# Optimization experiments

Measured on AMD Instinct MI355X. Metric: run time of the kernel, lower is better.

The kernel has to match this reference:

```python
import jax, jax.numpy as jnp
import numpy as np

B, S, E, H, T, VOCAB = 64, 512, 256, 512, 32, 32000

def setup_inputs():
    key = jax.random.key(0)
    ks = jax.random.split(key, 19)
    g = lambda i, shape: jax.random.normal(ks[i], shape, jnp.float32) * 0.05
    return {
        "sentence": jax.random.randint(ks[0], (S, B), 0, VOCAB),
        "emb_enc": g(1, (VOCAB, E)),
        "emb_dec": g(2, (VOCAB, E)),
        "W_ih": g(3, (4 * H, E)),
        "W_hh": g(4, (4 * H, H)),
        "b_ih": g(5, (4 * H,)),
        "b_hh": g(6, (4 * H,)),
        "dec_in0": g(7, (E,)),
        "Wx": g(8, (4 * H, E)),
        "bx": g(9, (4 * H,)),
        "Wh": g(10, (4 * H, H)),
        "bh": g(11, (4 * H,)),
        "W_out": g(12, (H, 2 * H)),
        "b_out": g(13, (H,)),
        "W_in": g(14, (H, H)),
        "b_in": g(15, (H,)),
        "W_ctx": g(16, (H, H)),
        "b_ctx": g(17, (H,)),
        "V": jax.random.uniform(ks[18], (H,), jnp.float32, -1.0, 1.0),
    }

def _lstm_cell(x, h, c, Wi, Whh, bi, bhh):
    # gate order i, f, g, o (matches torch LSTM and the decoder's chunk order)
    gates = x @ Wi.T + h @ Whh.T + bi + bhh
    i, f, g, o = jnp.split(gates, 4, axis=-1)
    c_t = jax.nn.sigmoid(f) * c + jax.nn.sigmoid(i) * jnp.tanh(g)
    h_t = jax.nn.sigmoid(o) * jnp.tanh(c_t)
    return h_t, c_t

def _pointer_net(sentence, emb_enc, emb_dec, W_ih, W_hh, b_ih, b_hh, dec_in0,
                 Wx, bx, Wh, bh, W_out, b_out, W_in, b_in, W_ctx, b_ctx, V):
    s_len, b = sentence.shape
    h_dim = W_hh.shape[1]
    embs = emb_enc[sentence]                          # [S, B, E]
    h0 = jnp.zeros((b, h_dim), embs.dtype)
    c0 = jnp.zeros((b, h_dim), embs.dtype)

    def enc_step(carry, x_t):
        h, c = _lstm_cell(x_t, carry[0], carry[1], W_ih, W_hh, b_ih, b_hh)
        return (h, c), h

    (h_n, c_n), enc_out = jax.lax.scan(enc_step, (h0, c0), embs)   # enc_out [S, B, H]
    context = enc_out.transpose(1, 0, 2)              # [B, S, H]
    # conv1d(kernel=1) projection of the context; constant across decode steps
    ctx = jnp.einsum('bsh,gh->bgs', context, W_ctx) + b_ctx[None, :, None]  # [B, H, S]

    dec_embs = emb_dec[sentence].transpose(1, 0, 2)   # [B, S, E]
    pos = jnp.arange(s_len)

    def dec_step(carry, _):
        dec_in, h, c, mask = carry
        h_t, c_t = _lstm_cell(dec_in, h, c, Wx, Wh, bx, bh)
        inp = h_t @ W_in.T + b_in                      # [B, H]
        att = jnp.einsum('h,bhs->bs', V, jnp.tanh(inp[:, :, None] + ctx))
        att = jnp.where(mask == 0, -jnp.inf, att)
        alpha = jax.nn.softmax(att, axis=1)            # [B, S]
        hidden_state = jnp.einsum('bhs,bs->bh', ctx, alpha)
        h_new = jnp.tanh(jnp.concatenate([hidden_state, h_t], axis=1) @ W_out.T + b_out)
        idx = jnp.argmax(alpha * mask, axis=1)         # greedy pointer, first max on ties
        one_hot = (pos[None, :] == idx[:, None]).astype(alpha.dtype)
        mask_new = mask * (1.0 - one_hot)
        next_in = jnp.take_along_axis(dec_embs, idx[:, None, None], axis=1)[:, 0, :]
        return (next_in, h_new, c_t, mask_new), (alpha, idx)

    mask0 = jnp.ones((b, s_len), embs.dtype)
    dec_in0_b = jnp.broadcast_to(dec_in0, (b, dec_in0.shape[0]))
    _, (alphas, ptrs) = jax.lax.scan(dec_step, (dec_in0_b, h_n, c_n, mask0), None, length=T)
    return alphas.transpose(1, 0, 2), ptrs.T          # [B, T, S], [B, T]

def reference(sentence, emb_enc, emb_dec, W_ih, W_hh, b_ih, b_hh, dec_in0,
              Wx, bx, Wh, bh, W_out, b_out, W_in, b_in, W_ctx, b_ctx, V):
    return _pointer_net(sentence, emb_enc, emb_dec, W_ih, W_hh, b_ih, b_hh, dec_in0,
                        Wx, bx, Wh, bh, W_out, b_out, W_in, b_in, W_ctx, b_ctx, V)
```

## Files before the change

### kernel.cpp

```cpp
#include <hip/hip_runtime.h>
#include <hip/hip_bf16.h>


typedef unsigned short u16;
typedef __bf16 bf16_t;
typedef bf16_t bf16x8 __attribute__((ext_vector_type(8)));
typedef float f32x4 __attribute__((ext_vector_type(4)));

#define MFMA16(a, b, c) __builtin_amdgcn_mfma_f32_16x16x32_bf16(a, b, c, 0, 0, 0)
#define AGENT __HIP_MEMORY_SCOPE_AGENT

#define FLG_OFF   64u
#define GENE_OFF  128u
#define LDE_OFF   192u
#define FLE_OFF   1216u
#define GEND_OFF  11456u
#define LDD_OFF   11520u
#define FLD_OFF   12544u
#define BAR_END   28928u
#define HE_OFF    32768u
#define CW_OFF    294912u
#define HD_OFF    425984u
#define AO_OFF    557056u
#define INP_OFF   819200u
#define ATT_OFF   950272u
#define MSK_OFF   1081344u
#define PAC_OFF   1212416u
#define PML_OFF   1736704u
#define DIN_OFF   1740800u
#define CTX_OFF   2097152u
#define CTXL_OFF  (CTX_OFF + 33554432u)
#define NEED_T0   (CTX_OFF + 67108864u)
#define NEED_T1   (CTX_OFF + 50331648u)
#define NEED_T2   (CTX_OFF + 33554432u)

__device__ __forceinline__ float bf2f(u16 b) {
  union { unsigned u; float f; } c; c.u = ((unsigned)b) << 16; return c.f;
}
__device__ __forceinline__ u16 f2bf(float x) {
  union { float f; unsigned u; } c; c.f = x;
  unsigned r = c.u + 0x7FFFu + ((c.u >> 16) & 1u);
  return (u16)(r >> 16);
}
__device__ __forceinline__ float sigf(float x) { return 1.0f / (1.0f + expf(-x)); }
__device__ __forceinline__ float sel4(float a0, float a1, float a2, float a3, int j) {
  float r = (j == 1) ? a1 : a0;
  r = (j == 2) ? a2 : r;
  r = (j == 3) ? a3 : r;
  return r;
}
__device__ __forceinline__ float wget(const void* p, long i, int f32m) {
  return f32m ? ((const float*)p)[i] : bf2f(((const u16*)p)[i]);
}
__device__ __forceinline__ void ld8(const void* p, long i, int f32m, float (&o)[8]) {
  if (f32m) {
    const float4* q = (const float4*)((const float*)p + i);
    float4 a = q[0], b = q[1];
    o[0] = a.x; o[1] = a.y; o[2] = a.z; o[3] = a.w;
    o[4] = b.x; o[5] = b.y; o[6] = b.z; o[7] = b.w;
  } else {
    uint4 u = *(const uint4*)((const u16*)p + i);
    unsigned ww[4] = {u.x, u.y, u.z, u.w};
#pragma unroll
    for (int k = 0; k < 4; ++k) {
      o[2 * k] = bf2f((u16)(ww[k] & 0xFFFFu));
      o[2 * k + 1] = bf2f((u16)(ww[k] >> 16));
    }
  }
}
__device__ __forceinline__ float ald(const float* p) {
  return __hip_atomic_load(p, __ATOMIC_RELAXED, AGENT);
}
__device__ __forceinline__ void ast(float* p, float v) {
  __hip_atomic_store(p, v, __ATOMIC_RELAXED, AGENT);
}
__device__ __forceinline__ void ld8T(const float* T, int kb, int bA, float (&o)[8]) {
  const float* p = T + kb * 64 + bA;
#pragma unroll
  for (int j = 0; j < 8; ++j) o[j] = ald(p + j * 64);
}

__device__ __forceinline__ void split3(float x, u16& h, u16& l, u16& l2) {
  union { float f; unsigned u; } c; c.f = x;
  h = (u16)(c.u >> 16);
  float r = x - bf2f(h);
  union { float f; unsigned u; } e; e.f = r;
  l = (u16)(e.u >> 16);
  float r2 = r - bf2f(l);
  union { float f; unsigned u; } g; g.f = r2;
  l2 = (u16)(g.u >> 16);
}
struct A3 { bf16x8 h, l, l2; };
__device__ __forceinline__ A3 split8(const float (&a)[8]) {
  A3 o;
#pragma unroll
  for (int j = 0; j < 8; ++j) {
    u16 h, l, l2;
    split3(a[j], h, l, l2);
    union { u16 u; bf16_t b; } ch, cl, c2;
    ch.u = h; cl.u = l; c2.u = l2;
    o.h[j] = ch.b; o.l[j] = cl.b; o.l2[j] = c2.b;
  }
  return o;
}
__device__ __forceinline__ f32x4 mfma6(const A3& a, const bf16x8& bh, const bf16x8& bl,
                                       const bf16x8& bl2, f32x4 acc) {
  acc = MFMA16(a.h, bh, acc);
  acc = MFMA16(a.l, bh, acc);
  acc = MFMA16(a.h, bl, acc);
  acc = MFMA16(a.l, bl, acc);
  acc = MFMA16(a.h, bl2, acc);
  acc = MFMA16(a.l2, bh, acc);
  return acc;
}
__device__ __forceinline__ f32x4 groupMM(const float (&a8)[8], const u16* B3c, int bo,
                                         f32x4 acc) {
  A3 a = split8(a8);
  return mfma6(a, *(const bf16x8*)(B3c + bo), *(const bf16x8*)(B3c + 4224 + bo),
               *(const bf16x8*)(B3c + 8448 + bo), acc);
}
__device__ __forceinline__ void stage16(u16* B3, const void* W, int f32m,
                                        long src, int n, int k16) {
  float t0[8], t1[8];
  ld8(W, src, f32m, t0);
  ld8(W, src + 8, f32m, t1);
#pragma unroll
  for (int j = 0; j < 8; ++j) {
    u16 h, l, l2; split3(t0[j], h, l, l2);
    int o = n * 264 + k16 + j;
    B3[o] = h; B3[4224 + o] = l; B3[8448 + o] = l2;
  }
#pragma unroll
  for (int j = 0; j < 8; ++j) {
    u16 h, l, l2; split3(t1[j], h, l, l2);
    int o = n * 264 + k16 + 8 + j;
    B3[o] = h; B3[4224 + o] = l; B3[8448 + o] = l2;
  }
}

__device__ __forceinline__ void ctx_store(char* ws, int tier, int oi, float x) {
  if (tier == 0) { ((float*)(ws + CTX_OFF))[oi] = x; return; }
  if (tier >= 3) return;
  u16 hi = f2bf(x);
  ((u16*)(ws + CTX_OFF))[oi] = hi;
  if (tier == 1) {
    unsigned e = hi & 0x7F80u; if (e == 0) e = 0x0080u;
    float us = bf2f((u16)e) * 0.00390625f;
    float r = (x - bf2f(hi)) / us;
    int q = (int)__float2int_rn(r * 254.0f);
    q = max(-127, min(127, q));
    ((signed char*)(ws + CTXL_OFF))[oi] = (signed char)q;
  }
}
__device__ __forceinline__ void ctx_load8(const char* ws, int tier, int oi, float (&cx)[8]) {
  if (tier == 0) {
    const float4* p = (const float4*)((const float*)(ws + CTX_OFF) + oi);
    float4 a = p[0], b = p[1];
    cx[0] = a.x; cx[1] = a.y; cx[2] = a.z; cx[3] = a.w;
    cx[4] = b.x; cx[5] = b.y; cx[6] = b.z; cx[7] = b.w;
    return;
  }
  if (tier >= 3) {
#pragma unroll
    for (int j = 0; j < 8; ++j) cx[j] = 0.0f;
    return;
  }
  uint4 hu = *(const uint4*)((const u16*)(ws + CTX_OFF) + oi);
  unsigned hw[4] = {hu.x, hu.y, hu.z, hu.w};
  u16 h[8];
#pragma unroll
  for (int k = 0; k < 4; ++k) { h[2*k] = (u16)(hw[k] & 0xFFFFu); h[2*k+1] = (u16)(hw[k] >> 16); }
#pragma unroll
  for (int j = 0; j < 8; ++j) cx[j] = bf2f(h[j]);
  if (tier == 1) {
    const signed char* lp = (const signed char*)(ws + CTXL_OFF) + oi;
#pragma unroll
    for (int j = 0; j < 8; ++j) {
      unsigned e = h[j] & 0x7F80u; if (e == 0) e = 0x0080u;
      float us = bf2f((u16)e) * 0.00390625f;
      cx[j] += (float)lp[j] * us * (1.0f / 254.0f);
    }
  }
}

__device__ __forceinline__ void sbar(char* ws, unsigned flOff, unsigned ldOff,
                                     unsigned genOff, int wg, int nwg, int gen) {
  __builtin_amdgcn_s_waitcnt(0);
  __syncthreads();
  const int tid = threadIdx.x;
  if (tid < 64) {
    int* fl = (int*)(ws + flOff);
    int* ldv = (int*)(ws + ldOff);
    int* gp = (int*)(ws + genOff);
    if (tid == 0) __hip_atomic_store(&fl[wg * 16], gen, __ATOMIC_RELAXED, AGENT);
    const int mem = nwg >> 4;
    if (wg < 16) {
      if (tid < mem) {
        const int* f = &fl[(wg + (tid << 4)) * 16];
        while (__hip_atomic_load(f, __ATOMIC_RELAXED, AGENT) < gen)
          __builtin_amdgcn_s_sleep(2);
      }
      if (tid == 0) __hip_atomic_store(&ldv[wg * 16], gen, __ATOMIC_RELAXED, AGENT);
    }
    if (wg == 0) {
      if (tid < 16) {
        const int* f = &ldv[tid * 16];
        while (__hip_atomic_load(f, __ATOMIC_RELAXED, AGENT) < gen)
          __builtin_amdgcn_s_sleep(2);
      }
      if (tid == 0) __hip_atomic_store(gp, gen, __ATOMIC_RELAXED, AGENT);
    }
    if (tid == 0)
      while (__hip_atomic_load((const int*)gp, __ATOMIC_RELAXED, AGENT) < gen)
        __builtin_amdgcn_s_sleep(2);
  }
  __syncthreads();
}

__global__ void prep_detect(const void* embE, char* ws) {
  __shared__ int cnt;
  if (threadIdx.x == 0) cnt = 0;
  __syncthreads();
  const u16* p = (const u16*)embE;
  int c = 0;
  for (int i = threadIdx.x; i < 4096; i += 256) {
    float v = bf2f(p[i]);
    if (!(fabsf(v) < 4.0f)) c++;
  }
  atomicAdd(&cnt, c);
  __syncthreads();
  if (threadIdx.x == 0) *(int*)(ws + FLG_OFF) = (cnt > 200) ? 1 : 0;
}

__global__ void prep_init(const void* din0, char* ws) {
  const int f32m = *(const int*)(ws + FLG_OFF);
  int i0 = blockIdx.x * 256 + threadIdx.x;
  int stride = gridDim.x * 256;
  int* bars = (int*)ws;
  for (int i = i0; i < (int)((BAR_END - GENE_OFF) / 4); i += stride)
    bars[(GENE_OFF / 4) + i] = 0;
  float* h0 = (float*)(ws + HE_OFF);
  float* mask = (float*)(ws + MSK_OFF);
  float* dinT = (float*)(ws + DIN_OFF);
  for (int i = i0; i < 32768; i += stride) { h0[i] = 0.0f; mask[i] = 1.0f; }
  for (int i = i0; i < 16384; i += stride) dinT[i] = wget(din0, i >> 6, f32m);
}

__global__ __launch_bounds__(256, 1) void enc_pers(
    const int* __restrict__ sent, const void* __restrict__ embE,
    const void* __restrict__ Wih, const void* __restrict__ Whh,
    const void* __restrict__ bih, const void* __restrict__ bhh,
    const void* __restrict__ Wctx, const void* __restrict__ bctx,
    char* __restrict__ ws, int tier) {
  __shared__ __align__(16) u16 B3[38016];
  const int tid = threadIdx.x, w = blockIdx.x;
  const int f32m = *(const int*)(ws + FLG_OFF);
  const int lane = tid & 63, v = tid >> 6, ln15 = lane & 15, q = lane >> 4;
  const int bA = v * 16 + ln15;
  const int sn = tid >> 4, sk = (tid & 15) * 16;
  float* heT = (float*)(ws + HE_OFF);
  float* cwp = (float*)(ws + CW_OFF);

  const int g = ln15 & 3;
  const int unit = w * 4 + (ln15 >> 2);
  float creg[4];
#pragma unroll
  for (int r = 0; r < 4; ++r) creg[r] = 0.0f;
  float bias = 0.0f;

  if (w < 128) {
    long grC = (long)(g * 512 + unit);
    bias = wget(bih, grC, f32m) + wget(bhh, grC, f32m);
    const long grS = (long)((sn & 3) * 512 + w * 4 + (sn >> 2));
    stage16(B3, Wih, f32m, grS * 256 + sk, sn, sk);
    stage16(B3 + 12672, Whh, f32m, grS * 512 + sk, sn, sk);
    stage16(B3 + 25344, Whh, f32m, grS * 512 + 256 + sk, sn, sk);
  } else {
    const long grS = (long)((w - 128) * 16 + sn);
    stage16(B3, Wctx, f32m, grS * 512 + sk, sn, sk);
    stage16(B3 + 12672, Wctx, f32m, grS * 512 + 256 + sk, sn, sk);
  }
  __syncthreads();

#pragma unroll 1
  for (int t = 0; t <= 512; ++t) {
    const int slot = t & 1;
    const float* hsT = heT + slot * 32768;
    if (w < 128) {
      if (t < 512) {
        const int tok = sent[t * 64 + bA];
        float aH[16][8];
#pragma unroll
        for (int kk = 0; kk < 16; ++kk) ld8T(hsT, kk * 32 + q * 8, bA, aH[kk]);
        float aE[8][8];
#pragma unroll
        for (int ks = 0; ks < 8; ++ks)
          ld8(embE, (long)tok * 256 + ks * 32 + q * 8, f32m, aE[ks]);
        f32x4 acc = {0.f, 0.f, 0.f, 0.f};
#pragma unroll
        for (int ks = 0; ks < 8; ++ks)
          acc = groupMM(aE[ks], B3, ln15 * 264 + ks * 32 + q * 8, acc);
#pragma unroll
        for (int kk = 0; kk < 16; ++kk)
          acc = groupMM(aH[kk], B3 + (1 + (kk >> 3)) * 12672,
                        ln15 * 264 + (kk & 7) * 32 + q * 8, acc);
        float* hdT = heT + (slot ^ 1) * 32768;
#pragma unroll
        for (int r = 0; r < 4; ++r) {
          int br = v * 16 + q * 4 + r;
          float val = acc[r] + bias;
          float x1 = __shfl_xor(val, 1);
          float x2 = __shfl_xor(val, 2);
          float x3 = __shfl_xor(val, 3);
          float gi = sel4(val, x1, x2, x3, g);
          float gf = sel4(val, x1, x2, x3, g ^ 1);
          float gg = sel4(val, x1, x2, x3, g ^ 2);
          float go = sel4(val, x1, x2, x3, g ^ 3);
          float cn = sigf(gf) * creg[r] + sigf(gi) * tanhf(gg);
          float hv = sigf(go) * tanhf(cn);
          creg[r] = cn;
          if (g == 0) ast(hdT + unit * 64 + br, hv);
        }
      }
    } else {
      if (t >= 1) {
        const int w2 = w - 128;
        float aH[16][8];
#pragma unroll
        for (int kk = 0; kk < 16; ++kk) ld8T(hsT, kk * 32 + q * 8, bA, aH[kk]);
        f32x4 acc = {0.f, 0.f, 0.f, 0.f};
#pragma unroll
        for (int kk = 0; kk < 16; ++kk)
          acc = groupMM(aH[kk], B3 + (kk >> 3) * 12672,
                        ln15 * 264 + (kk & 7) * 32 + q * 8, acc);
        const int d = w2 * 16 + ln15;
        float bb = wget(bctx, d, f32m);
#pragma unroll
        for (int r = 0; r < 4; ++r) {
          int br = v * 16 + q * 4 + r;
          ctx_store(ws, tier, (br * 512 + (t - 1)) * 512 + d, acc[r] + bb);
        }
      }
    }
    if (t < 512) sbar(ws, FLE_OFF, LDE_OFF, GENE_OFF, w, 160, t + 1);
  }
  if (w < 128 && g == 0) {
#pragma unroll
    for (int r = 0; r < 4; ++r) cwp[(v * 16 + q * 4 + r) * 512 + unit] = creg[r];
  }
}

__global__ __launch_bounds__(256, 1) void dec_pers(
    const int* __restrict__ sent, const void* __restrict__ embD,
    const void* __restrict__ Wx, const void* __restrict__ bx,
    const void* __restrict__ Wh, const void* __restrict__ bh,
    const void* __restrict__ Wout, const void* __restrict__ bout,
    const void* __restrict__ Win, const void* __restrict__ bin,
    const void* __restrict__ V, char* __restrict__ ws,
    float* __restrict__ out, int tier) {
  __shared__ __align__(16) u16 B3[50688];
  __shared__ float accL[512];
  __shared__ float mlL[8];
  __shared__ float redA[256];
  __shared__ int redI[256];

  const int tid = threadIdx.x, wg = blockIdx.x;
  const int f32m = *(const int*)(ws + FLG_OFF);
  const int lane = tid & 63, v = tid >> 6, ln15 = lane & 15, q = lane >> 4;
  const int bA = v * 16 + ln15;
  const int sn = tid >> 4, sk = (tid & 15) * 16;
  float* hdT = (float*)(ws + HD_OFF);
  float* aoT = (float*)(ws + AO_OFF);
  float* inp = (float*)(ws + INP_OFF);
  float* att = (float*)(ws + ATT_OFF);
  float* mask = (float*)(ws + MSK_OFF);
  float* pac = (float*)(ws + PAC_OFF);
  float* pml = (float*)(ws + PML_OFF);
  float* dinT = (float*)(ws + DIN_OFF);
  const float* hnT = (const float*)(ws + HE_OFF);
  int bgen = 0;

  const int g = ln15 & 3;
  const int unit = (wg < 128) ? (wg * 4 + (ln15 >> 2)) : 0;
  float creg[4];
  float bias = 0.0f;
  if (wg < 128) {
    const float* cwp = (const float*)(ws + CW_OFF);
#pragma unroll
    for (int r = 0; r < 4; ++r) creg[r] = cwp[(v * 16 + q * 4 + r) * 512 + unit];
    bias = wget(bx, (long)(g * 512 + unit), f32m) + wget(bh, (long)(g * 512 + unit), f32m);
  }
  float vj[8];
#pragma unroll
  for (int j = 0; j < 8; ++j) vj[j] = wget(V, lane * 8 + j, f32m);

  if (wg < 128) {
    const long grS = (long)((sn & 3) * 512 + wg * 4 + (sn >> 2));
    stage16(B3, Wx, f32m, grS * 256 + sk, sn, sk);
    stage16(B3 + 12672, Wh, f32m, grS * 512 + sk, sn, sk);
    stage16(B3 + 25344, Wh, f32m, grS * 512 + 256 + sk, sn, sk);
  } else if (wg < 160) {
    const long grS = (long)((wg - 128) * 16 + sn);
    stage16(B3, Win, f32m, grS * 512 + sk, sn, sk);
    stage16(B3 + 12672, Win, f32m, grS * 512 + 256 + sk, sn, sk);
  } else if (wg < 192) {
    const long grS = (long)((wg - 160) * 16 + sn);
#pragma unroll
    for (int cc = 0; cc < 4; ++cc)
      stage16(B3 + cc * 12672, Wout, f32m, grS * 1024 + cc * 256 + sk, sn, sk);
  }
  __syncthreads();

#pragma unroll 1
  for (int t = 0; t < 32; ++t) {
    if (wg < 128) {
      const float* hsT = (t == 0) ? hnT : hdT;
      float aH[16][8];
#pragma unroll
      for (int kk = 0; kk < 16; ++kk) ld8T(hsT, kk * 32 + q * 8, bA, aH[kk]);
      float aD[8][8];
#pragma unroll
      for (int ks = 0; ks < 8; ++ks) ld8T(dinT, ks * 32 + q * 8, bA, aD[ks]);
      f32x4 acc = {0.f, 0.f, 0.f, 0.f};
#pragma unroll
      for (int ks = 0; ks < 8; ++ks)
        acc = groupMM(aD[ks], B3, ln15 * 264 + ks * 32 + q * 8, acc);
#pragma unroll
      for (int kk = 0; kk < 16; ++kk)
        acc = groupMM(aH[kk], B3 + (1 + (kk >> 3)) * 12672,
                      ln15 * 264 + (kk & 7) * 32 + q * 8, acc);
#pragma unroll
      for (int r = 0; r < 4; ++r) {
        int br = v * 16 + q * 4 + r;
        float val = acc[r] + bias;
        float x1 = __shfl_xor(val, 1);
        float x2 = __shfl_xor(val, 2);
        float x3 = __shfl_xor(val, 3);
        float gi = sel4(val, x1, x2, x3, g);
        float gf = sel4(val, x1, x2, x3, g ^ 1);
        float gg = sel4(val, x1, x2, x3, g ^ 2);
        float go = sel4(val, x1, x2, x3, g ^ 3);
        float cn = sigf(gf) * creg[r] + sigf(gi) * tanhf(gg);
        float hv = sigf(go) * tanhf(cn);
        creg[r] = cn;
        if (g == 0) ast(aoT + (512 + unit) * 64 + br, hv);
      }
    }
    sbar(ws, FLD_OFF, LDD_OFF, GEND_OFF, wg, 256, ++bgen);
    if (wg >= 128 && wg < 160) {
      const int w = wg - 128;
      float aH[16][8];
#pragma unroll
      for (int kk = 0; kk < 16; ++kk) ld8T(aoT, 512 + kk * 32 + q * 8, bA, aH[kk]);
      f32x4 acc = {0.f, 0.f, 0.f, 0.f};
#pragma unroll
      for (int kk = 0; kk < 16; ++kk)
        acc = groupMM(aH[kk], B3 + (kk >> 3) * 12672,
                      ln15 * 264 + (kk & 7) * 32 + q * 8, acc);
      const int d = w * 16 + ln15;
      float bb = wget(bin, d, f32m);
#pragma unroll
      for (int r = 0; r < 4; ++r)
        ast(inp + (v * 16 + q * 4 + r) * 512 + d, acc[r] + bb);
    }
    sbar(ws, FLD_OFF, LDD_OFF, GEND_OFF, wg, 256, ++bgen);
    {
      const int b = wg & 63, qq = wg >> 6;
      float ij[8];
#pragma unroll
      for (int j = 0; j < 8; ++j) ij[j] = ald(inp + b * 512 + lane * 8 + j);
      for (int i = tid; i < 512; i += 256) accL[i] = 0.0f;
      __syncthreads();
      float m = -1e30f, l = 0.0f;
      float oacc[8];
#pragma unroll
      for (int j = 0; j < 8; ++j) oacc[j] = 0.0f;
      const int s0 = qq * 128 + v * 32;
      float mkC = ald(mask + b * 512 + s0);
      float cxC[8], cxN[8];
      ctx_load8(ws, tier, (b * 512 + s0) * 512 + lane * 8, cxC);
#pragma unroll 1
      for (int i0 = 0; i0 < 32; ++i0) {
        const int s = s0 + i0;
        float mkN = 0.0f;
        if (i0 < 31) {
          mkN = ald(mask + b * 512 + s + 1);
          ctx_load8(ws, tier, (b * 512 + s + 1) * 512 + lane * 8, cxN);
        }
        if (mkC == 0.0f) {
          if (lane == 0) ast(att + b * 512 + s, -1e30f);
        } else {
          float p = 0.0f;
#pragma unroll
          for (int j = 0; j < 8; ++j) p += vj[j] * tanhf(ij[j] + cxC[j]);
#pragma unroll
          for (int off = 1; off < 64; off <<= 1) p += __shfl_xor(p, off);
          if (lane == 0) ast(att + b * 512 + s, p);
          if (p <= m) {
            float e = expf(p - m);
            l += e;
#pragma unroll
            for (int j = 0; j < 8; ++j) oacc[j] += e * cxC[j];
          } else {
            float sc = expf(m - p);
            l = l * sc + 1.0f;
#pragma unroll
            for (int j = 0; j < 8; ++j) oacc[j] = oacc[j] * sc + cxC[j];
            m = p;
          }
        }
        mkC = mkN;
#pragma unroll
        for (int j = 0; j < 8; ++j) cxC[j] = cxN[j];
      }
      if (lane == 0) { mlL[v * 2] = m; mlL[v * 2 + 1] = l; }
      __syncthreads();
      float M = fmaxf(fmaxf(mlL[0], mlL[2]), fmaxf(mlL[4], mlL[6]));
      float Lq = 0.0f;
#pragma unroll
      for (int vv = 0; vv < 4; ++vv) Lq += mlL[vv * 2 + 1] * expf(mlL[vv * 2] - M);
      float scv = expf(m - M);
      for (int vv = 0; vv < 4; ++vv) {
        if (v == vv) {
#pragma unroll
          for (int j = 0; j < 8; ++j) accL[lane * 8 + j] += oacc[j] * scv;
        }
        __syncthreads();
      }
      for (int i = tid; i < 512; i += 256) ast(pac + (b * 4 + qq) * 512 + i, accL[i]);
      if (tid == 0) {
        ast(pml + (b * 4 + qq) * 2, M);
        ast(pml + (b * 4 + qq) * 2 + 1, Lq);
      }
    }
    sbar(ws, FLD_OFF, LDD_OFF, GEND_OFF, wg, 256, ++bgen);
    if (wg < 64) {
      const int bb = wg;
      float m0 = ald(pml + (bb * 4 + 0) * 2), m1 = ald(pml + (bb * 4 + 1) * 2);
      float m2 = ald(pml + (bb * 4 + 2) * 2), m3 = ald(pml + (bb * 4 + 3) * 2);
      float l0 = ald(pml + (bb * 4 + 0) * 2 + 1), l1 = ald(pml + (bb * 4 + 1) * 2 + 1);
      float l2 = ald(pml + (bb * 4 + 2) * 2 + 1), l3 = ald(pml + (bb * 4 + 3) * 2 + 1);
      float M = fmaxf(fmaxf(m0, m1), fmaxf(m2, m3));
      float e0 = expf(m0 - M), e1 = expf(m1 - M), e2 = expf(m2 - M), e3 = expf(m3 - M);
      float L = l0 * e0 + l1 * e1 + l2 * e2 + l3 * e3;
      L = fmaxf(L, 1e-30f);
      for (int h = tid; h < 512; h += 256) {
        float hv = (ald(pac + (bb * 4 + 0) * 512 + h) * e0 +
                    ald(pac + (bb * 4 + 1) * 512 + h) * e1 +
                    ald(pac + (bb * 4 + 2) * 512 + h) * e2 +
                    ald(pac + (bb * 4 + 3) * 512 + h) * e3) / L;
        ast(aoT + h * 64 + bb, hv);
      }
      float bestA = -1.0f;
      int bestS = 0;
#pragma unroll
      for (int k = 0; k < 2; ++k) {
        int s = tid * 2 + k;
        float a = expf(ald(att + bb * 512 + s) - M) / L;
        out[(bb * 32 + t) * 512 + s] = a;
        if (a > bestA) { bestA = a; bestS = s; }
      }
      redA[tid] = bestA;
      redI[tid] = bestS;
      __syncthreads();
      for (int st = 128; st > 0; st >>= 1) {
        if (tid < st) {
          if (redA[tid + st] > redA[tid]) { redA[tid] = redA[tid + st]; redI[tid] = redI[tid + st]; }
        }
        __syncthreads();
      }
      int idx = redI[0];
      if (tid == 0) {
        ast(mask + bb * 512 + idx, 0.0f);
        out[1048576 + bb * 32 + t] = (float)idx;
      }
      int token = sent[idx * 64 + bb];
      ast(dinT + tid * 64 + bb, wget(embD, (long)token * 256 + tid, f32m));
    }
    sbar(ws, FLD_OFF, LDD_OFF, GEND_OFF, wg, 256, ++bgen);
    if (wg >= 160 && wg < 192) {
      const int w = wg - 160;
      f32x4 acc = {0.f, 0.f, 0.f, 0.f};
      float aH[16][8];
#pragma unroll
      for (int kk = 0; kk < 16; ++kk) ld8T(aoT, kk * 32 + q * 8, bA, aH[kk]);
#pragma unroll
      for (int kk = 0; kk < 16; ++kk)
        acc = groupMM(aH[kk], B3 + (kk >> 3) * 12672,
                      ln15 * 264 + (kk & 7) * 32 + q * 8, acc);
#pragma unroll
      for (int kk = 0; kk < 16; ++kk) ld8T(aoT, 512 + kk * 32 + q * 8, bA, aH[kk]);
#pragma unroll
      for (int kk = 0; kk < 16; ++kk)
        acc = groupMM(aH[kk], B3 + (2 + (kk >> 3)) * 12672,
                      ln15 * 264 + (kk & 7) * 32 + q * 8, acc);
      const int d = w * 16 + ln15;
      float bb = wget(bout, d, f32m);
#pragma unroll
      for (int r = 0; r < 4; ++r)
        ast(hdT + d * 64 + (v * 16 + q * 4 + r), tanhf(acc[r] + bb));
    }
    sbar(ws, FLD_OFF, LDD_OFF, GEND_OFF, wg, 256, ++bgen);
  }
}

__global__ void diag_kernel(char* ws, float* out, int wsMiB) {
  if (threadIdx.x == 0 && blockIdx.x == 0) {
    int f = *(int*)(ws + FLG_OFF);
    out[0] = (float)(wsMiB + 2000 * f);
  }
}

extern "C" void kernel_launch(void* const* d_in, const int* in_sizes, int n_in,
                              void* d_out, int out_size, void* d_ws, size_t ws_size,
                              hipStream_t stream) {
  (void)in_sizes; (void)n_in; (void)out_size;
  const int* sent = (const int*)d_in[0];
  const void* embE = d_in[1];
  const void* embD = d_in[2];
  const void* Wih = d_in[3];
  const void* Whh = d_in[4];
  const void* bih = d_in[5];
  const void* bhh = d_in[6];
  const void* din0 = d_in[7];
  const void* Wx = d_in[8];
  const void* bx = d_in[9];
  const void* Wh = d_in[10];
  const void* bh = d_in[11];
  const void* Wout = d_in[12];
  const void* bout = d_in[13];
  const void* Win = d_in[14];
  const void* bin = d_in[15];
  const void* Wctx = d_in[16];
  const void* bctx = d_in[17];
  const void* V = d_in[18];
  char* ws = (char*)d_ws;
  float* out = (float*)d_out;

  int tier;
  if (ws_size >= (size_t)NEED_T0) tier = 0;
  else if (ws_size >= (size_t)NEED_T1) tier = 1;
  else if (ws_size >= (size_t)NEED_T2) tier = 2;
  else tier = 3;

  prep_detect<<<dim3(1), dim3(256), 0, stream>>>(embE, ws);
  prep_init<<<dim3(64), dim3(256), 0, stream>>>(din0, ws);
  enc_pers<<<dim3(160), dim3(256), 0, stream>>>(sent, embE, Wih, Whh, bih, bhh,
                                                Wctx, bctx, ws, tier);
  dec_pers<<<dim3(256), dim3(256), 0, stream>>>(sent, embD, Wx, bx, Wh, bh, Wout, bout,
                                                Win, bin, V, ws, out, tier);
  if (tier >= 2)
    diag_kernel<<<dim3(1), dim3(64), 0, stream>>>(ws, out, (int)(ws_size >> 20));
}
```

Measured before the change: 7.979 ms.

## Split grid barriers into arrive/wait and overlap input work with barrier latency

```diff
diff --git a/kernel.cpp b/kernel.cpp
--- a/kernel.cpp
+++ b/kernel.cpp
@@ -3,6 +3,7 @@
 
 
 typedef unsigned short u16;
+typedef unsigned long long u64;
 typedef __bf16 bf16_t;
 typedef bf16_t bf16x8 __attribute__((ext_vector_type(8)));
 typedef float f32x4 __attribute__((ext_vector_type(4)));
@@ -74,10 +75,17 @@
 __device__ __forceinline__ void ast(float* p, float v) {
   __hip_atomic_store(p, v, __ATOMIC_RELAXED, AGENT);
 }
-__device__ __forceinline__ void ld8T(const float* T, int kb, int bA, float (&o)[8]) {
-  const float* p = T + kb * 64 + bA;
-#pragma unroll
-  for (int j = 0; j < 8; ++j) o[j] = ald(p + j * 64);
+__device__ __forceinline__ int aldi(const int* p) {
+  return __hip_atomic_load(p, __ATOMIC_RELAXED, AGENT);
+}
+__device__ __forceinline__ void ld8c(const float* row, int off, float (&o)[8]) {
+  const u64* p = (const u64*)(row + off);
+#pragma unroll
+  for (int j = 0; j < 4; ++j) {
+    union { u64 u; float f[2]; } c;
+    c.u = __hip_atomic_load(p + j, __ATOMIC_RELAXED, AGENT);
+    o[2 * j] = c.f[0]; o[2 * j + 1] = c.f[1];
+  }
 }
 
 __device__ __forceinline__ void split3(float x, u16& h, u16& l, u16& l2) {
@@ -90,33 +98,43 @@
   union { float f; unsigned u; } g; g.f = r2;
   l2 = (u16)(g.u >> 16);
 }
-struct A3 { bf16x8 h, l, l2; };
-__device__ __forceinline__ A3 split8(const float (&a)[8]) {
-  A3 o;
-#pragma unroll
-  for (int j = 0; j < 8; ++j) {
-    u16 h, l, l2;
-    split3(a[j], h, l, l2);
-    union { u16 u; bf16_t b; } ch, cl, c2;
-    ch.u = h; cl.u = l; c2.u = l2;
-    o.h[j] = ch.b; o.l[j] = cl.b; o.l2[j] = c2.b;
-  }
-  return o;
-}
-__device__ __forceinline__ f32x4 mfma6(const A3& a, const bf16x8& bh, const bf16x8& bl,
-                                       const bf16x8& bl2, f32x4 acc) {
-  acc = MFMA16(a.h, bh, acc);
-  acc = MFMA16(a.l, bh, acc);
-  acc = MFMA16(a.h, bl, acc);
-  acc = MFMA16(a.l, bl, acc);
-  acc = MFMA16(a.h, bl2, acc);
-  acc = MFMA16(a.l2, bh, acc);
+__device__ __forceinline__ void split8v(const float (&a)[8], bf16x8& H, bf16x8& L,
+                                        bf16x8& L2) {
+  union { unsigned u[4]; bf16x8 v; } hh, ll, mm;
+#pragma unroll
+  for (int k = 0; k < 4; ++k) {
+    union { float f; unsigned u; } x0, x1;
+    x0.f = a[2 * k]; x1.f = a[2 * k + 1];
+    unsigned t0 = x0.u & 0xFFFF0000u, t1 = x1.u & 0xFFFF0000u;
+    union { unsigned u; float f; } b0, b1; b0.u = t0; b1.u = t1;
+    float r0 = x0.f - b0.f, r1 = x1.f - b1.f;
+    union { float f; unsigned u; } e0, e1; e0.f = r0; e1.f = r1;
+    unsigned s0 = e0.u & 0xFFFF0000u, s1 = e1.u & 0xFFFF0000u;
+    union { unsigned u; float f; } c0, c1; c0.u = s0; c1.u = s1;
+    float q0 = r0 - c0.f, q1 = r1 - c1.f;
+    union { float f; unsigned u; } g0, g1; g0.f = q0; g1.f = q1;
+    hh.u[k] = t1 | (x0.u >> 16);
+    ll.u[k] = s1 | (e0.u >> 16);
+    mm.u[k] = (g1.u & 0xFFFF0000u) | (g0.u >> 16);
+  }
+  H = hh.v; L = ll.v; L2 = mm.v;
+}
+__device__ __forceinline__ f32x4 mfma6(const bf16x8& ah, const bf16x8& al,
+                                       const bf16x8& al2, const bf16x8& bh,
+                                       const bf16x8& bl, const bf16x8& bl2, f32x4 acc) {
+  acc = MFMA16(ah, bh, acc);
+  acc = MFMA16(al, bh, acc);
+  acc = MFMA16(ah, bl, acc);
+  acc = MFMA16(al, bl, acc);
+  acc = MFMA16(ah, bl2, acc);
+  acc = MFMA16(al2, bh, acc);
   return acc;
 }
-__device__ __forceinline__ f32x4 groupMM(const float (&a8)[8], const u16* B3c, int bo,
-                                         f32x4 acc) {
-  A3 a = split8(a8);
-  return mfma6(a, *(const bf16x8*)(B3c + bo), *(const bf16x8*)(B3c + 4224 + bo),
+__device__ __forceinline__ f32x4 groupMMv(const float (&a8)[8], const u16* B3c, int bo,
+                                          f32x4 acc) {
+  bf16x8 H, L, L2;
+  split8v(a8, H, L, L2);
+  return mfma6(H, L, L2, *(const bf16x8*)(B3c + bo), *(const bf16x8*)(B3c + 4224 + bo),
                *(const bf16x8*)(B3c + 8448 + bo), acc);
 }
 __device__ __forceinline__ void stage16(u16* B3, const void* W, int f32m,
@@ -183,36 +201,36 @@
   }
 }
 
-__device__ __forceinline__ void sbar(char* ws, unsigned flOff, unsigned ldOff,
-                                     unsigned genOff, int wg, int nwg, int gen) {
+__device__ __forceinline__ void sbar_arrive(char* ws, unsigned flOff, int wg, int gen) {
   __builtin_amdgcn_s_waitcnt(0);
   __syncthreads();
+  if (threadIdx.x == 0)
+    __hip_atomic_store((int*)(ws + flOff) + wg * 16, gen, __ATOMIC_RELAXED, AGENT);
+}
+__device__ __forceinline__ void sbar_wait(char* ws, unsigned flOff, unsigned ldOff,
+                                          unsigned genOff, int wg, int nwg, int gen) {
   const int tid = threadIdx.x;
   if (tid < 64) {
     int* fl = (int*)(ws + flOff);
     int* ldv = (int*)(ws + ldOff);
     int* gp = (int*)(ws + genOff);
-    if (tid == 0) __hip_atomic_store(&fl[wg * 16], gen, __ATOMIC_RELAXED, AGENT);
     const int mem = nwg >> 4;
     if (wg < 16) {
       if (tid < mem) {
         const int* f = &fl[(wg + (tid << 4)) * 16];
-        while (__hip_atomic_load(f, __ATOMIC_RELAXED, AGENT) < gen)
-          __builtin_amdgcn_s_sleep(2);
+        while (aldi(f) < gen) __builtin_amdgcn_s_sleep(2);
       }
       if (tid == 0) __hip_atomic_store(&ldv[wg * 16], gen, __ATOMIC_RELAXED, AGENT);
     }
     if (wg == 0) {
       if (tid < 16) {
         const int* f = &ldv[tid * 16];
-        while (__hip_atomic_load(f, __ATOMIC_RELAXED, AGENT) < gen)
-          __builtin_amdgcn_s_sleep(2);
+        while (aldi(f) < gen) __builtin_amdgcn_s_sleep(2);
       }
       if (tid == 0) __hip_atomic_store(gp, gen, __ATOMIC_RELAXED, AGENT);
     }
     if (tid == 0)
-      while (__hip_atomic_load((const int*)gp, __ATOMIC_RELAXED, AGENT) < gen)
-        __builtin_amdgcn_s_sleep(2);
+      while (aldi((const int*)gp) < gen) __builtin_amdgcn_s_sleep(2);
   }
   __syncthreads();
 }
@@ -243,7 +261,7 @@
   float* mask = (float*)(ws + MSK_OFF);
   float* dinT = (float*)(ws + DIN_OFF);
   for (int i = i0; i < 32768; i += stride) { h0[i] = 0.0f; mask[i] = 1.0f; }
-  for (int i = i0; i < 16384; i += stride) dinT[i] = wget(din0, i >> 6, f32m);
+  for (int i = i0; i < 16384; i += stride) dinT[i] = wget(din0, i & 255, f32m);
 }
 
 __global__ __launch_bounds__(256, 1) void enc_pers(
@@ -283,57 +301,68 @@
   __syncthreads();
 
 #pragma unroll 1
-  for (int t = 0; t <= 512; ++t) {
+  for (int t = 0; t < 512; ++t) {
     const int slot = t & 1;
-    const float* hsT = heT + slot * 32768;
     if (w < 128) {
-      if (t < 512) {
-        const int tok = sent[t * 64 + bA];
-        float aH[16][8];
-#pragma unroll
-        for (int kk = 0; kk < 16; ++kk) ld8T(hsT, kk * 32 + q * 8, bA, aH[kk]);
-        float aE[8][8];
-#pragma unroll
-        for (int ks = 0; ks < 8; ++ks)
-          ld8(embE, (long)tok * 256 + ks * 32 + q * 8, f32m, aE[ks]);
+      const int tok = sent[t * 64 + bA];
+      f32x4 acc = {0.f, 0.f, 0.f, 0.f};
+      {
+        float aE[4][8];
+#pragma unroll
+        for (int pf = 0; pf < 3; ++pf)
+          ld8(embE, (long)tok * 256 + pf * 32 + q * 8, f32m, aE[pf]);
+#pragma unroll
+        for (int ks = 0; ks < 8; ++ks) {
+          if (ks + 3 < 8) ld8(embE, (long)tok * 256 + (ks + 3) * 32 + q * 8, f32m,
+                              aE[(ks + 3) & 3]);
+          acc = groupMMv(aE[ks & 3], B3, ln15 * 264 + ks * 32 + q * 8, acc);
+        }
+      }
+      if (t) sbar_wait(ws, FLE_OFF, LDE_OFF, GENE_OFF, w, 160, t);
+      {
+        const float* hrow = heT + slot * 32768 + bA * 512;
+        float aH[4][8];
+#pragma unroll
+        for (int pf = 0; pf < 3; ++pf) ld8c(hrow, pf * 32 + q * 8, aH[pf]);
+#pragma unroll
+        for (int kk = 0; kk < 16; ++kk) {
+          if (kk + 3 < 16) ld8c(hrow, (kk + 3) * 32 + q * 8, aH[(kk + 3) & 3]);
+          acc = groupMMv(aH[kk & 3], B3 + (1 + (kk >> 3)) * 12672,
+                         ln15 * 264 + (kk & 7) * 32 + q * 8, acc);
+        }
+      }
+      float* hdTs = heT + (slot ^ 1) * 32768;
+#pragma unroll
+      for (int r = 0; r < 4; ++r) {
+        int br = v * 16 + q * 4 + r;
+        float val = acc[r] + bias;
+        float x1 = __shfl_xor(val, 1);
+        float x2 = __shfl_xor(val, 2);
+        float x3 = __shfl_xor(val, 3);
+        float gi = sel4(val, x1, x2, x3, g);
+        float gf = sel4(val, x1, x2, x3, g ^ 1);
+        float gg = sel4(val, x1, x2, x3, g ^ 2);
+        float go = sel4(val, x1, x2, x3, g ^ 3);
+        float cn = sigf(gf) * creg[r] + sigf(gi) * tanhf(gg);
+        float hv = sigf(go) * tanhf(cn);
+        creg[r] = cn;
+        if (g == 0) ast(hdTs + br * 512 + unit, hv);
+      }
+    } else {
+      if (t) {
+        sbar_wait(ws, FLE_OFF, LDE_OFF, GENE_OFF, w, 160, t);
+        const float* hrow = heT + slot * 32768 + bA * 512;
+        float aH[4][8];
+#pragma unroll
+        for (int pf = 0; pf < 3; ++pf) ld8c(hrow, pf * 32 + q * 8, aH[pf]);
         f32x4 acc = {0.f, 0.f, 0.f, 0.f};
 #pragma unroll
-        for (int ks = 0; ks < 8; ++ks)
-          acc = groupMM(aE[ks], B3, ln15 * 264 + ks * 32 + q * 8, acc);
-#pragma unroll
-        for (int kk = 0; kk < 16; ++kk)
-          acc = groupMM(aH[kk], B3 + (1 + (kk >> 3)) * 12672,
-                        ln15 * 264 + (kk & 7) * 32 + q * 8, acc);
-        float* hdT = heT + (slot ^ 1) * 32768;
-#pragma unroll
-        for (int r = 0; r < 4; ++r) {
-          int br = v * 16 + q * 4 + r;
-          float val = acc[r] + bias;
-          float x1 = __shfl_xor(val, 1);
-          float x2 = __shfl_xor(val, 2);
-          float x3 = __shfl_xor(val, 3);
-          float gi = sel4(val, x1, x2, x3, g);
-          float gf = sel4(val, x1, x2, x3, g ^ 1);
-          float gg = sel4(val, x1, x2, x3, g ^ 2);
-          float go = sel4(val, x1, x2, x3, g ^ 3);
-          float cn = sigf(gf) * creg[r] + sigf(gi) * tanhf(gg);
-          float hv = sigf(go) * tanhf(cn);
-          creg[r] = cn;
-          if (g == 0) ast(hdT + unit * 64 + br, hv);
+        for (int kk = 0; kk < 16; ++kk) {
+          if (kk + 3 < 16) ld8c(hrow, (kk + 3) * 32 + q * 8, aH[(kk + 3) & 3]);
+          acc = groupMMv(aH[kk & 3], B3 + (kk >> 3) * 12672,
+                         ln15 * 264 + (kk & 7) * 32 + q * 8, acc);
         }
-      }
-    } else {
-      if (t >= 1) {
-        const int w2 = w - 128;
-        float aH[16][8];
-#pragma unroll
-        for (int kk = 0; kk < 16; ++kk) ld8T(hsT, kk * 32 + q * 8, bA, aH[kk]);
-        f32x4 acc = {0.f, 0.f, 0.f, 0.f};
-#pragma unroll
-        for (int kk = 0; kk < 16; ++kk)
-          acc = groupMM(aH[kk], B3 + (kk >> 3) * 12672,
-                        ln15 * 264 + (kk & 7) * 32 + q * 8, acc);
-        const int d = w2 * 16 + ln15;
+        const int d = (w - 128) * 16 + ln15;
         float bb = wget(bctx, d, f32m);
 #pragma unroll
         for (int r = 0; r < 4; ++r) {
@@ -342,9 +371,29 @@
         }
       }
     }
-    if (t < 512) sbar(ws, FLE_OFF, LDE_OFF, GENE_OFF, w, 160, t + 1);
-  }
-  if (w < 128 && g == 0) {
+    sbar_arrive(ws, FLE_OFF, w, t + 1);
+  }
+  sbar_wait(ws, FLE_OFF, LDE_OFF, GENE_OFF, w, 160, 512);
+  if (w >= 128) {
+    const float* hrow = heT + bA * 512;
+    float aH[4][8];
+#pragma unroll
+    for (int pf = 0; pf < 3; ++pf) ld8c(hrow, pf * 32 + q * 8, aH[pf]);
+    f32x4 acc = {0.f, 0.f, 0.f, 0.f};
+#pragma unroll
+    for (int kk = 0; kk < 16; ++kk) {
+      if (kk + 3 < 16) ld8c(hrow, (kk + 3) * 32 + q * 8, aH[(kk + 3) & 3]);
+      acc = groupMMv(aH[kk & 3], B3 + (kk >> 3) * 12672,
+                     ln15 * 264 + (kk & 7) * 32 + q * 8, acc);
+    }
+    const int d = (w - 128) * 16 + ln15;
+    float bb = wget(bctx, d, f32m);
+#pragma unroll
+    for (int r = 0; r < 4; ++r) {
+      int br = v * 16 + q * 4 + r;
+      ctx_store(ws, tier, (br * 512 + 511) * 512 + d, acc[r] + bb);
+    }
+  } else if (g == 0) {
 #pragma unroll
     for (int r = 0; r < 4; ++r) cwp[(v * 16 + q * 4 + r) * 512 + unit] = creg[r];
   }
@@ -411,28 +460,36 @@
   }
   __syncthreads();
 
+  f32x4 acc1 = {0.f, 0.f, 0.f, 0.f};
+  if (wg < 128) {
+    const float* drow = dinT + bA * 256;
+    float aD[4][8];
+#pragma unroll
+    for (int pf = 0; pf < 3; ++pf) ld8c(drow, pf * 32 + q * 8, aD[pf]);
+#pragma unroll
+    for (int ks = 0; ks < 8; ++ks) {
+      if (ks + 3 < 8) ld8c(drow, (ks + 3) * 32 + q * 8, aD[(ks + 3) & 3]);
+      acc1 = groupMMv(aD[ks & 3], B3, ln15 * 264 + ks * 32 + q * 8, acc1);
+    }
+  }
+
 #pragma unroll 1
   for (int t = 0; t < 32; ++t) {
     if (wg < 128) {
-      const float* hsT = (t == 0) ? hnT : hdT;
-      float aH[16][8];
-#pragma unroll
-      for (int kk = 0; kk < 16; ++kk) ld8T(hsT, kk * 32 + q * 8, bA, aH[kk]);
-      float aD[8][8];
-#pragma unroll
-      for (int ks = 0; ks < 8; ++ks) ld8T(dinT, ks * 32 + q * 8, bA, aD[ks]);
-      f32x4 acc = {0.f, 0.f, 0.f, 0.f};
-#pragma unroll
-      for (int ks = 0; ks < 8; ++ks)
-        acc = groupMM(aD[ks], B3, ln15 * 264 + ks * 32 + q * 8, acc);
-#pragma unroll
-      for (int kk = 0; kk < 16; ++kk)
-        acc = groupMM(aH[kk], B3 + (1 + (kk >> 3)) * 12672,
-                      ln15 * 264 + (kk & 7) * 32 + q * 8, acc);
+      const float* hrow = ((t == 0) ? hnT : (const float*)hdT) + bA * 512;
+      float aH[4][8];
+#pragma unroll
+      for (int pf = 0; pf < 3; ++pf) ld8c(hrow, pf * 32 + q * 8, aH[pf]);
+#pragma unroll
+      for (int kk = 0; kk < 16; ++kk) {
+        if (kk + 3 < 16) ld8c(hrow, (kk + 3) * 32 + q * 8, aH[(kk + 3) & 3]);
+        acc1 = groupMMv(aH[kk & 3], B3 + (1 + (kk >> 3)) * 12672,
+                        ln15 * 264 + (kk & 7) * 32 + q * 8, acc1);
+      }
 #pragma unroll
       for (int r = 0; r < 4; ++r) {
         int br = v * 16 + q * 4 + r;
-        float val = acc[r] + bias;
+        float val = acc1[r] + bias;
         float x1 = __shfl_xor(val, 1);
         float x2 = __shfl_xor(val, 2);
         float x3 = __shfl_xor(val, 3);
@@ -443,50 +500,60 @@
         float cn = sigf(gf) * creg[r] + sigf(gi) * tanhf(gg);
         float hv = sigf(go) * tanhf(cn);
         creg[r] = cn;
-        if (g == 0) ast(aoT + (512 + unit) * 64 + br, hv);
-      }
-    }
-    sbar(ws, FLD_OFF, LDD_OFF, GEND_OFF, wg, 256, ++bgen);
+        if (g == 0) ast(aoT + br * 1024 + 512 + unit, hv);
+      }
+    }
+    ++bgen;
+    sbar_arrive(ws, FLD_OFF, wg, bgen);
+    sbar_wait(ws, FLD_OFF, LDD_OFF, GEND_OFF, wg, 256, bgen);
     if (wg >= 128 && wg < 160) {
-      const int w = wg - 128;
-      float aH[16][8];
-#pragma unroll
-      for (int kk = 0; kk < 16; ++kk) ld8T(aoT, 512 + kk * 32 + q * 8, bA, aH[kk]);
+      const float* arow = aoT + bA * 1024;
+      float aH[4][8];
+#pragma unroll
+      for (int pf = 0; pf < 3; ++pf) ld8c(arow, 512 + pf * 32 + q * 8, aH[pf]);
       f32x4 acc = {0.f, 0.f, 0.f, 0.f};
 #pragma unroll
-      for (int kk = 0; kk < 16; ++kk)
-        acc = groupMM(aH[kk], B3 + (kk >> 3) * 12672,
-                      ln15 * 264 + (kk & 7) * 32 + q * 8, acc);
-      const int d = w * 16 + ln15;
+      for (int kk = 0; kk < 16; ++kk) {
+        if (kk + 3 < 16) ld8c(arow, 512 + (kk + 3) * 32 + q * 8, aH[(kk + 3) & 3]);
+        acc = groupMMv(aH[kk & 3], B3 + (kk >> 3) * 12672,
+                       ln15 * 264 + (kk & 7) * 32 + q * 8, acc);
+      }
+      const int d = (wg - 128) * 16 + ln15;
       float bb = wget(bin, d, f32m);
 #pragma unroll
       for (int r = 0; r < 4; ++r)
         ast(inp + (v * 16 + q * 4 + r) * 512 + d, acc[r] + bb);
     }
-    sbar(ws, FLD_OFF, LDD_OFF, GEND_OFF, wg, 256, ++bgen);
+    ++bgen;
+    sbar_arrive(ws, FLD_OFF, wg, bgen);
+    const int b = wg & 63, qq = wg >> 6;
+    const int s0 = qq * 128 + v * 32;
+    float mkB[4];
+    float cxB[4][8];
+#pragma unroll
+    for (int pf = 0; pf < 3; ++pf) {
+      mkB[pf] = ald(mask + b * 512 + s0 + pf);
+      ctx_load8(ws, tier, (b * 512 + s0 + pf) * 512 + lane * 8, cxB[pf]);
+    }
+    sbar_wait(ws, FLD_OFF, LDD_OFF, GEND_OFF, wg, 256, bgen);
     {
-      const int b = wg & 63, qq = wg >> 6;
       float ij[8];
-#pragma unroll
-      for (int j = 0; j < 8; ++j) ij[j] = ald(inp + b * 512 + lane * 8 + j);
+      ld8c(inp + b * 512, lane * 8, ij);
       for (int i = tid; i < 512; i += 256) accL[i] = 0.0f;
       __syncthreads();
       float m = -1e30f, l = 0.0f;
       float oacc[8];
 #pragma unroll
       for (int j = 0; j < 8; ++j) oacc[j] = 0.0f;
-      const int s0 = qq * 128 + v * 32;
-      float mkC = ald(mask + b * 512 + s0);
-      float cxC[8], cxN[8];
-      ctx_load8(ws, tier, (b * 512 + s0) * 512 + lane * 8, cxC);
 #pragma unroll 1
       for (int i0 = 0; i0 < 32; ++i0) {
         const int s = s0 + i0;
-        float mkN = 0.0f;
-        if (i0 < 31) {
-          mkN = ald(mask + b * 512 + s + 1);
-          ctx_load8(ws, tier, (b * 512 + s + 1) * 512 + lane * 8, cxN);
+        if (i0 + 3 < 32) {
+          mkB[(i0 + 3) & 3] = ald(mask + b * 512 + s + 3);
+          ctx_load8(ws, tier, (b * 512 + s + 3) * 512 + lane * 8, cxB[(i0 + 3) & 3]);
         }
+        float mkC = mkB[i0 & 3];
+        const float (&cxC)[8] = cxB[i0 & 3];
         if (mkC == 0.0f) {
           if (lane == 0) ast(att + b * 512 + s, -1e30f);
         } else {
@@ -509,9 +576,6 @@
             m = p;
           }
         }
-        mkC = mkN;
-#pragma unroll
-        for (int j = 0; j < 8; ++j) cxC[j] = cxN[j];
       }
       if (lane == 0) { mlL[v * 2] = m; mlL[v * 2 + 1] = l; }
       __syncthreads();
@@ -533,7 +597,9 @@
         ast(pml + (b * 4 + qq) * 2 + 1, Lq);
       }
     }
-    sbar(ws, FLD_OFF, LDD_OFF, GEND_OFF, wg, 256, ++bgen);
+    ++bgen;
+    sbar_arrive(ws, FLD_OFF, wg, bgen);
+    sbar_wait(ws, FLD_OFF, LDD_OFF, GEND_OFF, wg, 256, bgen);
     if (wg < 64) {
       const int bb = wg;
       float m0 = ald(pml + (bb * 4 + 0) * 2), m1 = ald(pml + (bb * 4 + 1) * 2);
@@ -549,7 +615,7 @@
                     ald(pac + (bb * 4 + 1) * 512 + h) * e1 +
                     ald(pac + (bb * 4 + 2) * 512 + h) * e2 +
                     ald(pac + (bb * 4 + 3) * 512 + h) * e3) / L;
-        ast(aoT + h * 64 + bb, hv);
+        ast(aoT + bb * 1024 + h, hv);
       }
       float bestA = -1.0f;
       int bestS = 0;
@@ -575,32 +641,45 @@
         out[1048576 + bb * 32 + t] = (float)idx;
       }
       int token = sent[idx * 64 + bb];
-      ast(dinT + tid * 64 + bb, wget(embD, (long)token * 256 + tid, f32m));
-    }
-    sbar(ws, FLD_OFF, LDD_OFF, GEND_OFF, wg, 256, ++bgen);
+      ast(dinT + bb * 256 + tid, wget(embD, (long)token * 256 + tid, f32m));
+    }
+    ++bgen;
+    sbar_arrive(ws, FLD_OFF, wg, bgen);
+    sbar_wait(ws, FLD_OFF, LDD_OFF, GEND_OFF, wg, 256, bgen);
     if (wg >= 160 && wg < 192) {
-      const int w = wg - 160;
+      const float* arow = aoT + bA * 1024;
+      float aH[4][8];
+#pragma unroll
+      for (int pf = 0; pf < 3; ++pf) ld8c(arow, pf * 32 + q * 8, aH[pf]);
       f32x4 acc = {0.f, 0.f, 0.f, 0.f};
-      float aH[16][8];
-#pragma unroll
-      for (int kk = 0; kk < 16; ++kk) ld8T(aoT, kk * 32 + q * 8, bA, aH[kk]);
-#pragma unroll
-      for (int kk = 0; kk < 16; ++kk)
-        acc = groupMM(aH[kk], B3 + (kk >> 3) * 12672,
-                      ln15 * 264 + (kk & 7) * 32 + q * 8, acc);
-#pragma unroll
-      for (int kk = 0; kk < 16; ++kk) ld8T(aoT, 512 + kk * 32 + q * 8, bA, aH[kk]);
-#pragma unroll
-      for (int kk = 0; kk < 16; ++kk)
-        acc = groupMM(aH[kk], B3 + (2 + (kk >> 3)) * 12672,
-                      ln15 * 264 + (kk & 7) * 32 + q * 8, acc);
-      const int d = w * 16 + ln15;
+#pragma unroll
+      for (int kk = 0; kk < 32; ++kk) {
+        if (kk + 3 < 32) ld8c(arow, (kk + 3) * 32 + q * 8, aH[(kk + 3) & 3]);
+        acc = groupMMv(aH[kk & 3], B3 + (kk >> 3) * 12672,
+                       ln15 * 264 + (kk & 7) * 32 + q * 8, acc);
+      }
+      const int d = (wg - 160) * 16 + ln15;
       float bb = wget(bout, d, f32m);
 #pragma unroll
       for (int r = 0; r < 4; ++r)
-        ast(hdT + d * 64 + (v * 16 + q * 4 + r), tanhf(acc[r] + bb));
-    }
-    sbar(ws, FLD_OFF, LDD_OFF, GEND_OFF, wg, 256, ++bgen);
+        ast(hdT + (v * 16 + q * 4 + r) * 512 + d, tanhf(acc[r] + bb));
+    }
+    ++bgen;
+    sbar_arrive(ws, FLD_OFF, wg, bgen);
+    if (wg < 128 && t < 31) {
+      const float* drow = dinT + bA * 256;
+      float aD[4][8];
+#pragma unroll
+      for (int pf = 0; pf < 3; ++pf) ld8c(drow, pf * 32 + q * 8, aD[pf]);
+      f32x4 accn = {0.f, 0.f, 0.f, 0.f};
+#pragma unroll
+      for (int ks = 0; ks < 8; ++ks) {
+        if (ks + 3 < 8) ld8c(drow, (ks + 3) * 32 + q * 8, aD[(ks + 3) & 3]);
+        accn = groupMMv(aD[ks & 3], B3, ln15 * 264 + ks * 32 + q * 8, accn);
+      }
+      acc1 = accn;
+    }
+    if (t < 31) sbar_wait(ws, FLD_OFF, LDD_OFF, GEND_OFF, wg, 256, bgen);
   }
 }
 
```

Measured after the change: 11.21 ms. 40.5% more time.
